# Kernel optimization log

Measured on AMD Instinct MI355X. Metric: run time of the kernel, lower is better.

The kernel has to match this reference:

```python
import jax, jax.numpy as jnp
import numpy as np

B, I, H, O = 256, 4096, 4096, 4096

def setup_inputs() -> dict:
    key = jax.random.key(0)
    ks = jax.random.split(key, 8)
    s_ih = 1.0 / np.sqrt(H)
    return {
        "x": jax.random.normal(ks[0], (B, I), jnp.float32),
        "h0": jax.random.normal(ks[1], (1, B, H), jnp.float32),
        "w_ih": jax.random.uniform(ks[2], (H, I), jnp.float32, -s_ih, s_ih),
        "b_ih": jax.random.uniform(ks[3], (H,), jnp.float32, -s_ih, s_ih),
        "w_hh": jax.random.uniform(ks[4], (H, H), jnp.float32, -s_ih, s_ih),
        "b_hh": jax.random.uniform(ks[5], (H,), jnp.float32, -s_ih, s_ih),
        "w_lin": jax.random.uniform(ks[6], (O, H), jnp.float32, -s_ih, s_ih),
        "b_lin": jax.random.uniform(ks[7], (O,), jnp.float32, -s_ih, s_ih),
    }

def reference(x, h0, w_ih, b_ih, w_hh, b_hh, w_lin, b_lin):
    # Single-step Elman RNN cell (seq_len=1, num_layers=1):
    # h' = tanh(x @ W_ih^T + b_ih + h @ W_hh^T + b_hh)
    h = h0[0]                                   # [B, H]
    hn = jnp.tanh(x @ w_ih.T + b_ih + h @ w_hh.T + b_hh)  # [B, H]
    logits = hn @ w_lin.T + b_lin               # [B, O]
    probs = jax.nn.softmax(logits, axis=-1)
    # rr has leading seq dim of 1; hn keeps [num_layers, B, H]
    return probs[None, :, :], hn[None, :, :]
```

## Files before the change

### kernel.cpp

```cpp
#include <hip/hip_runtime.h>
#include <hip/hip_bf16.h>
#include <cstdint>


using short8 = __attribute__((ext_vector_type(8))) short;
using f32x4  = __attribute__((ext_vector_type(4))) float;

#define HDIM 4096

__device__ __forceinline__ short bfbits(float f) {
    __bf16 b = (__bf16)f;
    return __builtin_bit_cast(short, b);
}
__device__ __forceinline__ short8 pack8(f32x4 a, f32x4 b) {
    short8 r;
    r[0] = bfbits(a[0]); r[1] = bfbits(a[1]); r[2] = bfbits(a[2]); r[3] = bfbits(a[3]);
    r[4] = bfbits(b[0]); r[5] = bfbits(b[1]); r[6] = bfbits(b[2]); r[7] = bfbits(b[3]);
    return r;
}

__device__ __forceinline__ void gld_lds16(const float* g, const float* l) {
    __builtin_amdgcn_global_load_lds(
        (const __attribute__((address_space(1))) void*)g,
        (__attribute__((address_space(3))) void*)l, 16, 0, 0);
}

template<int MODE>
__global__ __launch_bounds__(512) void rnn_gemm(
    const float* __restrict__ A0, const float* __restrict__ W0,
    const float* __restrict__ A1, const float* __restrict__ W1,
    float* __restrict__ out, int steps, int kslice)
{
    __shared__ __align__(16) float smem[16384];

    const int t    = threadIdx.x;
    const int lane = t & 63;
    const int wid  = t >> 6;
    const int bid  = blockIdx.x;
    const int grp   = bid & 7;
    const int ntile = bid >> 3;
    const int mtile = grp >> 2;
    const int ks    = grp & 3;
    const int m0 = mtile * 128, n0 = ntile * 128;
    const int wr = (wid & 3) * 32;
    const int wc = (wid >> 2) * 64;
    const int lr = lane & 15;
    const int lk = lane >> 4;

    const float* As; const float* Ws; int koff;
    if (MODE == 0) {
        if (ks < 2) { As = A0; Ws = W0; koff = ks * kslice; }
        else        { As = A1; Ws = W1; koff = (ks - 2) * kslice; }
    } else { As = A0; Ws = W0; koff = ks * kslice; }

    const int srow = lane >> 3;
    const int gc   = (lane & 7) ^ srow;

    auto stage = [&](int b, int step) {
        const int kb = koff + step * 32 + gc * 4;
        const float* lA = &smem[b * 8192 + wid * 512];
        const float* lB = &smem[b * 8192 + 4096 + wid * 512];
#pragma unroll
        for (int i = 0; i < 2; ++i) {
            const int row = wid * 16 + i * 8 + srow;
            gld_lds16(As + (size_t)(m0 + row) * HDIM + kb, lA + i * 256);
            gld_lds16(Ws + (size_t)(n0 + row) * HDIM + kb, lB + i * 256);
        }
    };

    f32x4 acc[2][4];
#pragma unroll
    for (int i = 0; i < 2; ++i)
#pragma unroll
        for (int j = 0; j < 4; ++j) acc[i][j] = (f32x4){0.f, 0.f, 0.f, 0.f};

    auto compute = [&](int b) {
        const float* Ab = &smem[b * 8192];
        const float* Bb = &smem[b * 8192 + 4096];
        short8 af[2], bf[4];
#pragma unroll
        for (int mr = 0; mr < 2; ++mr) {
            const int r = wr + mr * 16 + lr;
            const float* rp = Ab + r * 32;
            f32x4 lo = *(const f32x4*)(rp + ((2 * lk)     ^ (r & 7)) * 4);
            f32x4 hi = *(const f32x4*)(rp + ((2 * lk + 1) ^ (r & 7)) * 4);
            af[mr] = pack8(lo, hi);
        }
#pragma unroll
        for (int nr = 0; nr < 4; ++nr) {
            const int r = wc + nr * 16 + lr;
            const float* rp = Bb + r * 32;
            f32x4 lo = *(const f32x4*)(rp + ((2 * lk)     ^ (r & 7)) * 4);
            f32x4 hi = *(const f32x4*)(rp + ((2 * lk + 1) ^ (r & 7)) * 4);
            bf[nr] = pack8(lo, hi);
        }
#pragma unroll
        for (int mr = 0; mr < 2; ++mr)
#pragma unroll
            for (int nr = 0; nr < 4; ++nr)
                acc[mr][nr] = __builtin_amdgcn_mfma_f32_16x16x32_bf16(
                    af[mr], bf[nr], acc[mr][nr], 0, 0, 0);
    };

    stage(0, 0);
    stage(1, 1);
    asm volatile("s_waitcnt vmcnt(4)" ::: "memory");
    __builtin_amdgcn_s_barrier();
    __builtin_amdgcn_sched_barrier(0);
    for (int tt = 0; tt < steps; ++tt) {
        compute(tt & 1);
        __builtin_amdgcn_s_barrier();
        __builtin_amdgcn_sched_barrier(0);
        if (tt + 2 < steps) {
            stage(tt & 1, tt + 2);
            asm volatile("s_waitcnt vmcnt(4)" ::: "memory");
        } else {
            asm volatile("s_waitcnt vmcnt(0)" ::: "memory");
        }
        __builtin_amdgcn_s_barrier();
        __builtin_amdgcn_sched_barrier(0);
    }

#pragma unroll
    for (int mr = 0; mr < 2; ++mr)
#pragma unroll
        for (int nr = 0; nr < 4; ++nr) {
            const int n = n0 + wc + nr * 16 + lr;
#pragma unroll
            for (int e = 0; e < 4; ++e) {
                const int m = m0 + wr + mr * 16 + lk * 4 + e;
                atomicAdd(&out[(size_t)m * HDIM + n], acc[mr][nr][e]);
            }
        }
}

__global__ __launch_bounds__(256) void finish_hn(
    float* __restrict__ hn, const float* __restrict__ b_ih,
    const float* __restrict__ b_hh)
{
    const int idx = blockIdx.x * 256 + threadIdx.x;
    const int col = (idx & 1023) * 4;
    f32x4 v  = *((const f32x4*)hn + idx);
    f32x4 bi = *(const f32x4*)(b_ih + col);
    f32x4 bh = *(const f32x4*)(b_hh + col);
#pragma unroll
    for (int j = 0; j < 4; ++j) v[j] = tanhf(v[j] + bi[j] + bh[j]);
    *((f32x4*)hn + idx) = v;
}

__global__ __launch_bounds__(256) void softmax_bias(
    float* __restrict__ p, const float* __restrict__ bl)
{
    const int row = blockIdx.x;
    float* rp = p + (size_t)row * HDIM;
    const int t = threadIdx.x;

    f32x4 v[4];
#pragma unroll
    for (int i = 0; i < 4; ++i) {
        const int c = t + i * 256;
        v[i] = *(const f32x4*)(rp + c * 4);
        f32x4 b = *(const f32x4*)(bl + c * 4);
        v[i] += b;
    }

    float mx = -1e30f;
#pragma unroll
    for (int i = 0; i < 4; ++i)
#pragma unroll
        for (int j = 0; j < 4; ++j) mx = fmaxf(mx, v[i][j]);
#pragma unroll
    for (int off = 32; off; off >>= 1) mx = fmaxf(mx, __shfl_xor(mx, off));

    __shared__ float red[4];
    if ((t & 63) == 0) red[t >> 6] = mx;
    __syncthreads();
    mx = fmaxf(fmaxf(red[0], red[1]), fmaxf(red[2], red[3]));

    float sum = 0.f;
#pragma unroll
    for (int i = 0; i < 4; ++i)
#pragma unroll
        for (int j = 0; j < 4; ++j) {
            float e = __expf(v[i][j] - mx);
            v[i][j] = e;
            sum += e;
        }
#pragma unroll
    for (int off = 32; off; off >>= 1) sum += __shfl_xor(sum, off);

    __syncthreads();
    if ((t & 63) == 0) red[t >> 6] = sum;
    __syncthreads();
    sum = (red[0] + red[1]) + (red[2] + red[3]);

    const float inv = 1.f / sum;
#pragma unroll
    for (int i = 0; i < 4; ++i) {
        f32x4 o = v[i];
#pragma unroll
        for (int j = 0; j < 4; ++j) o[j] *= inv;
        *(f32x4*)(rp + (t + i * 256) * 4) = o;
    }
}

extern "C" void kernel_launch(void* const* d_in, const int* in_sizes, int n_in,
                              void* d_out, int out_size, void* d_ws, size_t ws_size,
                              hipStream_t stream) {
    const float* x     = (const float*)d_in[0];
    const float* h0    = (const float*)d_in[1];
    const float* w_ih  = (const float*)d_in[2];
    const float* b_ih  = (const float*)d_in[3];
    const float* w_hh  = (const float*)d_in[4];
    const float* b_hh  = (const float*)d_in[5];
    const float* w_lin = (const float*)d_in[6];
    const float* b_lin = (const float*)d_in[7];

    float* probs = (float*)d_out;
    float* hn    = (float*)d_out + 256 * HDIM;

    hipMemsetAsync(d_out, 0, (size_t)2 * 256 * HDIM * sizeof(float), stream);

    rnn_gemm<0><<<256, 512, 0, stream>>>(x, w_ih, h0, w_hh, hn, 64, 2048);
    finish_hn<<<1024, 256, 0, stream>>>(hn, b_ih, b_hh);
    rnn_gemm<1><<<256, 512, 0, stream>>>(hn, w_lin, nullptr, nullptr, probs, 32, 1024);
    softmax_bias<<<256, 256, 0, stream>>>(probs, b_lin);
}
```

Measured before the change: 270.6 us.

## Stage tiles through registers with bf16 conversion before LDS, doubling K per step

Replaces direct global-to-LDS fp32 loads with register-staged global loads that are converted to bf16 once and written into a swizzled LDS layout. Each pipeline step now covers 64 K elements instead of 32, halving the step count and barrier overhead. Conversion happens once per element instead of in every wave that reads it, and LDS traffic per step shrinks. It costs more registers for the two prefetch register sets and depends on the manual vmcnt/lgkmcnt waits being correct.

```diff
diff --git a/kernel.cpp b/kernel.cpp
--- a/kernel.cpp
+++ b/kernel.cpp
@@ -12,17 +12,11 @@
     __bf16 b = (__bf16)f;
     return __builtin_bit_cast(short, b);
 }
-__device__ __forceinline__ short8 pack8(f32x4 a, f32x4 b) {
+__device__ __forceinline__ short8 pack8(const float4& a, const float4& b) {
     short8 r;
-    r[0] = bfbits(a[0]); r[1] = bfbits(a[1]); r[2] = bfbits(a[2]); r[3] = bfbits(a[3]);
-    r[4] = bfbits(b[0]); r[5] = bfbits(b[1]); r[6] = bfbits(b[2]); r[7] = bfbits(b[3]);
+    r[0] = bfbits(a.x); r[1] = bfbits(a.y); r[2] = bfbits(a.z); r[3] = bfbits(a.w);
+    r[4] = bfbits(b.x); r[5] = bfbits(b.y); r[6] = bfbits(b.z); r[7] = bfbits(b.w);
     return r;
-}
-
-__device__ __forceinline__ void gld_lds16(const float* g, const float* l) {
-    __builtin_amdgcn_global_load_lds(
-        (const __attribute__((address_space(1))) void*)g,
-        (__attribute__((address_space(3))) void*)l, 16, 0, 0);
 }
 
 template<int MODE>
@@ -31,7 +25,7 @@
     const float* __restrict__ A1, const float* __restrict__ W1,
     float* __restrict__ out, int steps, int kslice)
 {
-    __shared__ __align__(16) float smem[16384];
+    __shared__ __align__(16) unsigned char smem[65536];
 
     const int t    = threadIdx.x;
     const int lane = t & 63;
@@ -53,73 +47,94 @@
         else        { As = A1; Ws = W1; koff = (ks - 2) * kslice; }
     } else { As = A0; Ws = W0; koff = ks * kslice; }
 
-    const int srow = lane >> 3;
-    const int gc   = (lane & 7) ^ srow;
-
-    auto stage = [&](int b, int step) {
-        const int kb = koff + step * 32 + gc * 4;
-        const float* lA = &smem[b * 8192 + wid * 512];
-        const float* lB = &smem[b * 8192 + 4096 + wid * 512];
-#pragma unroll
-        for (int i = 0; i < 2; ++i) {
-            const int row = wid * 16 + i * 8 + srow;
-            gld_lds16(As + (size_t)(m0 + row) * HDIM + kb, lA + i * 256);
-            gld_lds16(Ws + (size_t)(n0 + row) * HDIM + kb, lB + i * 256);
+    const int lr8 = lane >> 3;
+    const int ch  = lane & 7;
+    const int rbase = wid * 16;
+
+    float4 pa0, pa1, pa2, pa3, pb0, pb1, pb2, pb3;
+    float4 qa0, qa1, qa2, qa3, qb0, qb1, qb2, qb3;
+
+#define ISSUE(A0r, A1r, A2r, A3r, B0r, B1r, B2r, B3r, step)                     \
+    {                                                                           \
+        const int kb = koff + (step) * 64 + ch * 8;                             \
+        const float* ap = As + (size_t)(m0 + rbase + lr8) * HDIM + kb;          \
+        const float* wp = Ws + (size_t)(n0 + rbase + lr8) * HDIM + kb;          \
+        A0r = *(const float4*)(ap);            A1r = *(const float4*)(ap + 4);  \
+        A2r = *(const float4*)(ap + 8 * HDIM); A3r = *(const float4*)(ap + 8 * HDIM + 4); \
+        B0r = *(const float4*)(wp);            B1r = *(const float4*)(wp + 4);  \
+        B2r = *(const float4*)(wp + 8 * HDIM); B3r = *(const float4*)(wp + 8 * HDIM + 4); \
+    }
+
+#define WRITEBUF(A0r, A1r, A2r, A3r, B0r, B1r, B2r, B3r, b)                     \
+    {                                                                           \
+        unsigned char* base = smem + (b) * 32768;                               \
+        const int r0 = rbase + lr8, r1 = rbase + 8 + lr8;                       \
+        const int o0 = r0 * 128 + ((ch ^ (r0 & 7)) * 16);                       \
+        const int o1 = r1 * 128 + ((ch ^ (r1 & 7)) * 16);                       \
+        *(short8*)(base + o0)         = pack8(A0r, A1r);                        \
+        *(short8*)(base + o1)         = pack8(A2r, A3r);                        \
+        *(short8*)(base + 16384 + o0) = pack8(B0r, B1r);                        \
+        *(short8*)(base + 16384 + o1) = pack8(B2r, B3r);                        \
+    }
+
+    f32x4 acc[2][4];
+#pragma unroll
+    for (int i = 0; i < 2; ++i)
+#pragma unroll
+        for (int j = 0; j < 4; ++j) acc[i][j] = (f32x4){0.f, 0.f, 0.f, 0.f};
+
+    auto compute = [&](int b) {
+        const unsigned char* base = smem + b * 32768;
+#pragma unroll
+        for (int s = 0; s < 2; ++s) {
+            short8 af[2], bv[4];
+#pragma unroll
+            for (int mr = 0; mr < 2; ++mr) {
+                const int r = wr + mr * 16 + lr;
+                af[mr] = *(const short8*)(base + r * 128 + (((s * 4 + lk) ^ (r & 7)) * 16));
+            }
+#pragma unroll
+            for (int nr = 0; nr < 4; ++nr) {
+                const int r = wc + nr * 16 + lr;
+                bv[nr] = *(const short8*)(base + 16384 + r * 128 + (((s * 4 + lk) ^ (r & 7)) * 16));
+            }
+#pragma unroll
+            for (int mr = 0; mr < 2; ++mr)
+#pragma unroll
+                for (int nr = 0; nr < 4; ++nr)
+                    acc[mr][nr] = __builtin_amdgcn_mfma_f32_16x16x32_bf16(
+                        af[mr], bv[nr], acc[mr][nr], 0, 0, 0);
         }
     };
 
-    f32x4 acc[2][4];
-#pragma unroll
-    for (int i = 0; i < 2; ++i)
-#pragma unroll
-        for (int j = 0; j < 4; ++j) acc[i][j] = (f32x4){0.f, 0.f, 0.f, 0.f};
-
-    auto compute = [&](int b) {
-        const float* Ab = &smem[b * 8192];
-        const float* Bb = &smem[b * 8192 + 4096];
-        short8 af[2], bf[4];
-#pragma unroll
-        for (int mr = 0; mr < 2; ++mr) {
-            const int r = wr + mr * 16 + lr;
-            const float* rp = Ab + r * 32;
-            f32x4 lo = *(const f32x4*)(rp + ((2 * lk)     ^ (r & 7)) * 4);
-            f32x4 hi = *(const f32x4*)(rp + ((2 * lk + 1) ^ (r & 7)) * 4);
-            af[mr] = pack8(lo, hi);
-        }
-#pragma unroll
-        for (int nr = 0; nr < 4; ++nr) {
-            const int r = wc + nr * 16 + lr;
-            const float* rp = Bb + r * 32;
-            f32x4 lo = *(const f32x4*)(rp + ((2 * lk)     ^ (r & 7)) * 4);
-            f32x4 hi = *(const f32x4*)(rp + ((2 * lk + 1) ^ (r & 7)) * 4);
-            bf[nr] = pack8(lo, hi);
-        }
-#pragma unroll
-        for (int mr = 0; mr < 2; ++mr)
-#pragma unroll
-            for (int nr = 0; nr < 4; ++nr)
-                acc[mr][nr] = __builtin_amdgcn_mfma_f32_16x16x32_bf16(
-                    af[mr], bf[nr], acc[mr][nr], 0, 0, 0);
-    };
-
-    stage(0, 0);
-    stage(1, 1);
-    asm volatile("s_waitcnt vmcnt(4)" ::: "memory");
+    ISSUE(pa0, pa1, pa2, pa3, pb0, pb1, pb2, pb3, 0);
+    ISSUE(qa0, qa1, qa2, qa3, qb0, qb1, qb2, qb3, 1);
+    asm volatile("s_waitcnt vmcnt(8)" ::: "memory");
+    WRITEBUF(pa0, pa1, pa2, pa3, pb0, pb1, pb2, pb3, 0);
+    asm volatile("s_waitcnt lgkmcnt(0)" ::: "memory");
     __builtin_amdgcn_s_barrier();
-    __builtin_amdgcn_sched_barrier(0);
-    for (int tt = 0; tt < steps; ++tt) {
-        compute(tt & 1);
+
+    for (int tt = 0; tt < steps; tt += 2) {
+        if (tt + 2 < steps) ISSUE(pa0, pa1, pa2, pa3, pb0, pb1, pb2, pb3, tt + 2);
+        compute(0);
+        if (tt + 2 < steps) { asm volatile("s_waitcnt vmcnt(8)" ::: "memory"); }
+        else                { asm volatile("s_waitcnt vmcnt(0)" ::: "memory"); }
+        WRITEBUF(qa0, qa1, qa2, qa3, qb0, qb1, qb2, qb3, 1);
+        asm volatile("s_waitcnt lgkmcnt(0)" ::: "memory");
         __builtin_amdgcn_s_barrier();
-        __builtin_amdgcn_sched_barrier(0);
+
+        if (tt + 3 < steps) ISSUE(qa0, qa1, qa2, qa3, qb0, qb1, qb2, qb3, tt + 3);
+        compute(1);
         if (tt + 2 < steps) {
-            stage(tt & 1, tt + 2);
-            asm volatile("s_waitcnt vmcnt(4)" ::: "memory");
-        } else {
-            asm volatile("s_waitcnt vmcnt(0)" ::: "memory");
+            if (tt + 3 < steps) { asm volatile("s_waitcnt vmcnt(8)" ::: "memory"); }
+            else                { asm volatile("s_waitcnt vmcnt(0)" ::: "memory"); }
+            WRITEBUF(pa0, pa1, pa2, pa3, pb0, pb1, pb2, pb3, 0);
+            asm volatile("s_waitcnt lgkmcnt(0)" ::: "memory");
         }
         __builtin_amdgcn_s_barrier();
-        __builtin_amdgcn_sched_barrier(0);
-    }
+    }
+#undef ISSUE
+#undef WRITEBUF
 
 #pragma unroll
     for (int mr = 0; mr < 2; ++mr)
@@ -221,8 +236,8 @@
 
     hipMemsetAsync(d_out, 0, (size_t)2 * 256 * HDIM * sizeof(float), stream);
 
-    rnn_gemm<0><<<256, 512, 0, stream>>>(x, w_ih, h0, w_hh, hn, 64, 2048);
+    rnn_gemm<0><<<256, 512, 0, stream>>>(x, w_ih, h0, w_hh, hn, 32, 2048);
     finish_hn<<<1024, 256, 0, stream>>>(hn, b_ih, b_hh);
-    rnn_gemm<1><<<256, 512, 0, stream>>>(hn, w_lin, nullptr, nullptr, probs, 32, 1024);
+    rnn_gemm<1><<<256, 512, 0, stream>>>(hn, w_lin, nullptr, nullptr, probs, 16, 1024);
     softmax_bias<<<256, 256, 0, stream>>>(probs, b_lin);
 }
```

Result: faster. 261.9 us (-3.2%).
